# Kernel tuning notes

Hardware: AMD Instinct MI355X
Metric: run time of the kernel (lower is better)

Reference implementation:

```python
import jax, jax.numpy as jnp
import numpy as np

N_NODES = 40000
N_EDGES = 640000
N_GRAPHS = 256


def gcn_conv(x, W, b, src, dst, deg_inv_sqrt):
    # GCNConv: D^{-1/2} (A + I) D^{-1/2} X W + b
    h = (x @ W) * deg_inv_sqrt[:, None]          # pre-scale by norm of source
    agg = jax.ops.segment_sum(h[src], dst, num_segments=x.shape[0])
    agg = agg + h                                 # self-loop contribution
    return agg * deg_inv_sqrt[:, None] + b


def setup_inputs() -> dict:
    key = jax.random.key(0)
    ks = jax.random.split(key, 12)
    x = jax.random.normal(ks[0], (N_NODES, 128), dtype=jnp.float32)
    edge_index = jax.random.randint(ks[1], (2, N_EDGES), 0, N_NODES, dtype=jnp.int64)
    batch = jnp.sort(jax.random.randint(ks[2], (N_NODES,), 0, N_GRAPHS, dtype=jnp.int64))

    def glorot(k, shape):
        lim = float(np.sqrt(6.0 / (shape[0] + shape[1])))
        return jax.random.uniform(k, shape, jnp.float32, -lim, lim)

    return {
        "x": x,
        "W1": glorot(ks[3], (128, 128)), "b1": jnp.zeros((128,), jnp.float32),
        "W2": glorot(ks[4], (128, 64)),  "b2": jnp.zeros((64,), jnp.float32),
        "W3": glorot(ks[5], (64, 32)),   "b3": jnp.zeros((32,), jnp.float32),
        "Wl": glorot(ks[6], (32, 768)),  "bl": jnp.zeros((768,), jnp.float32),
        "edge_index": edge_index,
        "batch": batch,
    }


def reference(x, W1, b1, W2, b2, W3, b3, Wl, bl, edge_index, batch):
    n = x.shape[0]
    src, dst = edge_index[0], edge_index[1]
    # degree including self-loop (PyG gcn_norm with add_self_loops=True)
    deg = jax.ops.segment_sum(jnp.ones_like(dst, dtype=x.dtype), dst, num_segments=n) + 1.0
    dis = jax.lax.rsqrt(deg)

    h = jax.nn.relu(gcn_conv(x, W1, b1, src, dst, dis))
    h = jax.nn.relu(gcn_conv(h, W2, b2, src, dst, dis))
    h = jax.nn.relu(gcn_conv(h, W3, b3, src, dst, dis))

    # global mean pool per graph
    counts = jax.ops.segment_sum(jnp.ones((n,), x.dtype), batch, num_segments=N_GRAPHS)
    pooled = jax.ops.segment_sum(h, batch, num_segments=N_GRAPHS)
    pooled = pooled / jnp.maximum(counts, 1.0)[:, None]

    out = pooled @ Wl + bl                        # [B, 768]
    return out.reshape(N_GRAPHS, 48, 16)          # [B, 3*S^2, c]
```

## Files before the change

kernel.cpp:

```cpp
#include <hip/hip_runtime.h>
#include <hip/hip_fp16.h>


#define MAXSLOT 64

struct H8 { __half2 a, b, c, d; };

__device__ inline void acc_h8(float* acc, const H8& v) {
    float2 f;
    f = __half22float2(v.a); acc[0] += f.x; acc[1] += f.y;
    f = __half22float2(v.b); acc[2] += f.x; acc[3] += f.y;
    f = __half22float2(v.c); acc[4] += f.x; acc[5] += f.y;
    f = __half22float2(v.d); acc[6] += f.x; acc[7] += f.y;
}

__global__ void bucket_fill_kernel(const int* __restrict__ src, const int* __restrict__ dst,
                                   int* __restrict__ cursor, unsigned short* __restrict__ slots,
                                   int E) {
    int e = blockIdx.x * blockDim.x + threadIdx.x;
    if (e < E) {
        const int d = dst[e];
        const int pos = atomicAdd(&cursor[d], 1);
        if (pos < MAXSLOT) slots[(size_t)d * MAXSLOT + pos] = (unsigned short)src[e];
    }
}

template <int K, int C, int NR, bool HALF_IN>
__global__ __launch_bounds__(256, 4) void gemm_kernel(
        const void* __restrict__ x_, const float* __restrict__ W,
        const int* __restrict__ cursor, __half* __restrict__ h, int N) {
    constexpr int TC     = C / 8;
    constexpr int TN     = 256 / TC;
    constexpr int NPB    = NR * TN;
    constexpr int KSTAGE = 32;
    constexpr int XROW   = KSTAGE + 4;
    constexpr int WROW   = TC * 12;
    __shared__ __align__(16) float Xs[NPB * XROW];
    __shared__ __align__(16) float Ws[KSTAGE * WROW];

    const int tc = threadIdx.x % TC;
    const int tn = threadIdx.x / TC;
    const int c0 = tc * 8;
    const int nBase = blockIdx.x * NPB;
    const int n0 = nBase + tn * NR;

    float acc[NR][8] = {};

#pragma unroll 1
    for (int ks = 0; ks < K; ks += KSTAGE) {
        for (int idx = threadIdx.x; idx < KSTAGE * (C / 4); idx += 256) {
            const int k  = idx / (C / 4);
            const int f4 = idx % (C / 4);
            const int t  = f4 >> 1;
            const int hh = f4 & 1;
            *reinterpret_cast<float4*>(&Ws[k * WROW + t * 12 + hh * 4]) =
                *reinterpret_cast<const float4*>(&W[(size_t)(ks + k) * C + t * 8 + hh * 4]);
        }
        if (HALF_IN) {
            const __half* xh = (const __half*)x_;
            for (int idx = threadIdx.x; idx < NPB * (KSTAGE / 8); idx += 256) {
                const int row = idx / (KSTAGE / 8);
                const int c8  = (idx % (KSTAGE / 8)) * 8;
                const int nn  = nBase + row;
                float f[8];
                if (nn < N) {
                    const H8 v = *reinterpret_cast<const H8*>(&xh[(size_t)nn * K + ks + c8]);
                    float2 t2;
                    t2 = __half22float2(v.a); f[0] = t2.x; f[1] = t2.y;
                    t2 = __half22float2(v.b); f[2] = t2.x; f[3] = t2.y;
                    t2 = __half22float2(v.c); f[4] = t2.x; f[5] = t2.y;
                    t2 = __half22float2(v.d); f[6] = t2.x; f[7] = t2.y;
                } else {
#pragma unroll
                    for (int j = 0; j < 8; ++j) f[j] = 0.0f;
                }
                *reinterpret_cast<float4*>(&Xs[row * XROW + c8])     = *reinterpret_cast<float4*>(&f[0]);
                *reinterpret_cast<float4*>(&Xs[row * XROW + c8 + 4]) = *reinterpret_cast<float4*>(&f[4]);
            }
        } else {
            const float* xf = (const float*)x_;
            for (int idx = threadIdx.x; idx < NPB * (KSTAGE / 4); idx += 256) {
                const int row = idx / (KSTAGE / 4);
                const int c4  = (idx % (KSTAGE / 4)) * 4;
                const int nn  = nBase + row;
                const float4 v = (nn < N)
                    ? *reinterpret_cast<const float4*>(&xf[(size_t)nn * K + ks + c4])
                    : float4{0.f, 0.f, 0.f, 0.f};
                *reinterpret_cast<float4*>(&Xs[row * XROW + c4]) = v;
            }
        }
        __syncthreads();

#pragma unroll 2
        for (int k = 0; k < KSTAGE; k += 4) {
            float4 xv[NR];
#pragma unroll
            for (int i = 0; i < NR; ++i)
                xv[i] = *reinterpret_cast<const float4*>(&Xs[(tn * NR + i) * XROW + k]);
#pragma unroll
            for (int kk = 0; kk < 4; ++kk) {
                float wv[8];
                *reinterpret_cast<float4*>(&wv[0]) =
                    *reinterpret_cast<const float4*>(&Ws[(k + kk) * WROW + tc * 12]);
                *reinterpret_cast<float4*>(&wv[4]) =
                    *reinterpret_cast<const float4*>(&Ws[(k + kk) * WROW + tc * 12 + 4]);
#pragma unroll
                for (int i = 0; i < NR; ++i) {
                    const float xs = (&xv[i].x)[kk];
#pragma unroll
                    for (int j = 0; j < 8; ++j) acc[i][j] = fmaf(xs, wv[j], acc[i][j]);
                }
            }
        }
        __syncthreads();
    }

#pragma unroll
    for (int i = 0; i < NR; ++i) {
        const int nn = n0 + i;
        if (nn < N) {
            const float d = rsqrtf((float)cursor[nn] + 1.0f);
            H8 o;
            o.a = __floats2half2_rn(acc[i][0] * d, acc[i][1] * d);
            o.b = __floats2half2_rn(acc[i][2] * d, acc[i][3] * d);
            o.c = __floats2half2_rn(acc[i][4] * d, acc[i][5] * d);
            o.d = __floats2half2_rn(acc[i][6] * d, acc[i][7] * d);
            *reinterpret_cast<H8*>(&h[(size_t)nn * C + c0]) = o;
        }
    }
}

template <int C>
__global__ void gather_kernel(const __half* __restrict__ h, const int* __restrict__ cursor,
                              const unsigned short* __restrict__ slots,
                              const float* __restrict__ b, __half* __restrict__ outp, int N) {
    constexpr int CQ = C / 8;
    const long long tid = (long long)blockIdx.x * blockDim.x + threadIdx.x;
    const int node = (int)(tid / CQ);
    const int q    = (int)(tid % CQ);
    if (node >= N) return;

    const int degc = min(cursor[node], MAXSLOT);
    const unsigned short* sl = &slots[(size_t)node * MAXSLOT];

    float acc[8] = {};
    acc_h8(acc, *reinterpret_cast<const H8*>(&h[(size_t)node * C + q * 8]));

    int i = 0;
    for (; i + 8 <= degc; i += 8) {
        int s[8];
#pragma unroll
        for (int u = 0; u < 8; ++u) s[u] = sl[i + u];
        H8 v[8];
#pragma unroll
        for (int u = 0; u < 8; ++u) v[u] = *reinterpret_cast<const H8*>(&h[(size_t)s[u] * C + q * 8]);
#pragma unroll
        for (int u = 0; u < 8; ++u) acc_h8(acc, v[u]);
    }
    for (; i < degc; ++i) {
        const int s = sl[i];
        acc_h8(acc, *reinterpret_cast<const H8*>(&h[(size_t)s * C + q * 8]));
    }

    const float d = rsqrtf((float)cursor[node] + 1.0f);
    float r[8];
#pragma unroll
    for (int j = 0; j < 8; ++j) {
        float v = fmaf(acc[j], d, b[q * 8 + j]);
        r[j] = v > 0.0f ? v : 0.0f;
    }
    H8 o;
    o.a = __floats2half2_rn(r[0], r[1]);
    o.b = __floats2half2_rn(r[2], r[3]);
    o.c = __floats2half2_rn(r[4], r[5]);
    o.d = __floats2half2_rn(r[6], r[7]);
    *reinterpret_cast<H8*>(&outp[(size_t)node * C + q * 8]) = o;
}

__global__ __launch_bounds__(256) void gatherpoolhead_kernel(
        const __half* __restrict__ h, const int* __restrict__ cursor,
        const unsigned short* __restrict__ slots, const float* __restrict__ b3,
        const int* __restrict__ batch,
        const float* __restrict__ Wl, const float* __restrict__ bl,
        float* __restrict__ out, int N) {
    constexpr int C = 32;
    const int g = blockIdx.x;
    __shared__ int bounds[2];
    __shared__ __align__(16) float red[64 * 33];
    __shared__ float p[32];

    if (threadIdx.x == 0) {
        int lo = 0, hi = N;
        while (lo < hi) { int m = (lo + hi) >> 1; if (batch[m] <  g) lo = m + 1; else hi = m; }
        bounds[0] = lo;
        int lo2 = lo, hi2 = N;
        while (lo2 < hi2) { int m = (lo2 + hi2) >> 1; if (batch[m] <= g) lo2 = m + 1; else hi2 = m; }
        bounds[1] = lo2;
    }
    __syncthreads();
    const int lo = bounds[0], hi = bounds[1];

    const int q  = threadIdx.x & 3;
    const int nl = threadIdx.x >> 2;

    float pool[8] = {};
    for (int n = lo + nl; n < hi; n += 64) {
        const int degc = min(cursor[n], MAXSLOT);
        const unsigned short* sl = &slots[(size_t)n * MAXSLOT];

        float acc[8] = {};
        acc_h8(acc, *reinterpret_cast<const H8*>(&h[(size_t)n * C + q * 8]));
        int i = 0;
        for (; i + 4 <= degc; i += 4) {
            const int s0 = sl[i], s1 = sl[i + 1], s2 = sl[i + 2], s3 = sl[i + 3];
            const H8 v0 = *reinterpret_cast<const H8*>(&h[(size_t)s0 * C + q * 8]);
            const H8 v1 = *reinterpret_cast<const H8*>(&h[(size_t)s1 * C + q * 8]);
            const H8 v2 = *reinterpret_cast<const H8*>(&h[(size_t)s2 * C + q * 8]);
            const H8 v3 = *reinterpret_cast<const H8*>(&h[(size_t)s3 * C + q * 8]);
            acc_h8(acc, v0); acc_h8(acc, v1); acc_h8(acc, v2); acc_h8(acc, v3);
        }
        for (; i < degc; ++i) {
            const int s = sl[i];
            acc_h8(acc, *reinterpret_cast<const H8*>(&h[(size_t)s * C + q * 8]));
        }
        const float d = rsqrtf((float)cursor[n] + 1.0f);
#pragma unroll
        for (int j = 0; j < 8; ++j) {
            float v = fmaf(acc[j], d, b3[q * 8 + j]);
            pool[j] += v > 0.0f ? v : 0.0f;
        }
    }

#pragma unroll
    for (int j = 0; j < 8; ++j) red[nl * 33 + q * 8 + j] = pool[j];
    __syncthreads();
    for (int s = 32; s > 0; s >>= 1) {
        if (nl < s) {
#pragma unroll
            for (int j = 0; j < 8; ++j)
                red[nl * 33 + q * 8 + j] += red[(nl + s) * 33 + q * 8 + j];
        }
        __syncthreads();
    }
    if (threadIdx.x < 32) {
        float cnt = (float)(hi - lo);
        cnt = cnt < 1.0f ? 1.0f : cnt;
        p[threadIdx.x] = red[threadIdx.x] / cnt;
    }
    __syncthreads();

    for (int j = threadIdx.x; j < 768; j += 256) {
        float a = bl[j];
#pragma unroll
        for (int k = 0; k < 32; ++k) a = fmaf(p[k], Wl[k * 768 + j], a);
        out[g * 768 + j] = a;
    }
}


extern "C" void kernel_launch(void* const* d_in, const int* in_sizes, int n_in,
                              void* d_out, int out_size, void* d_ws, size_t ws_size,
                              hipStream_t stream) {
    const float* x   = (const float*)d_in[0];
    const float* W1  = (const float*)d_in[1];
    const float* b1  = (const float*)d_in[2];
    const float* W2  = (const float*)d_in[3];
    const float* b2  = (const float*)d_in[4];
    const float* W3  = (const float*)d_in[5];
    const float* b3  = (const float*)d_in[6];
    const float* Wl  = (const float*)d_in[7];
    const float* bl  = (const float*)d_in[8];
    const int* ei    = (const int*)d_in[9];
    const int* batch = (const int*)d_in[10];

    const int N = in_sizes[0] / 128;
    const int E = in_sizes[9] / 2;
    const int G = out_size / 768;

    const int* src = ei;
    const int* dst = ei + E;
    float* out = (float*)d_out;

    __half* H              = (__half*)d_ws;
    __half* A              = H + (size_t)N * 128;
    __half* Bb             = A + (size_t)N * 128;
    int* cursor            = (int*)(Bb + (size_t)N * 64);
    unsigned short* slots  = (unsigned short*)(cursor + N);

    hipMemsetAsync(cursor, 0, (size_t)N * sizeof(int), stream);
    bucket_fill_kernel<<<(E + 255) / 256, 256, 0, stream>>>(src, dst, cursor, slots, E);

    gemm_kernel<128, 128, 4, false><<<(N + 63) / 64, 256, 0, stream>>>(x, W1, cursor, H, N);
    gather_kernel<128><<<(int)(((long long)N * 16 + 255) / 256), 256, 0, stream>>>(
        H, cursor, slots, b1, A, N);

    gemm_kernel<128, 64, 2, true><<<(N + 63) / 64, 256, 0, stream>>>(A, W2, cursor, H, N);
    gather_kernel<64><<<(int)(((long long)N * 8 + 255) / 256), 256, 0, stream>>>(
        H, cursor, slots, b2, Bb, N);

    gemm_kernel<64, 32, 2, true><<<(N + 127) / 128, 256, 0, stream>>>(Bb, W3, cursor, H, N);

    gatherpoolhead_kernel<<<G, 256, 0, stream>>>(H, cursor, slots, b3, batch, Wl, bl, out, N);
}
```

Baseline: 240.4 us.

## Fuse bucket fill with layer-1 GEMM and fuse gathers with following GEMMs

Edge bucketing and the first X·W1 GEMM now share a single launch, with block ranges split between the two jobs. Because the degree is no longer known when the GEMM runs, the source normalization moves into the layer-1 gather as a per-neighbor rsqrt. The layer-1 and layer-2 gathers are fused with the next layer's small GEMM through shared-memory rows, which removes the intermediate activation round-trips to global memory and two launches. The slot table is halved to 32 entries and backed by a global overflow list that high-degree nodes scan linearly; this also makes the code handle degrees above the old cap correctly. The costs are extra per-neighbor cursor reads and a weaker per-thread GEMM inside the fused kernels.

```diff
diff --git a/kernel.cpp b/kernel.cpp
--- a/kernel.cpp
+++ b/kernel.cpp
@@ -2,7 +2,8 @@
 #include <hip/hip_fp16.h>
 
 
-#define MAXSLOT 64
+#define MAXSLOT 32
+#define OVFCAP  8192
 
 struct H8 { __half2 a, b, c, d; };
 
@@ -13,90 +14,75 @@
     f = __half22float2(v.c); acc[4] += f.x; acc[5] += f.y;
     f = __half22float2(v.d); acc[6] += f.x; acc[7] += f.y;
 }
-
-__global__ void bucket_fill_kernel(const int* __restrict__ src, const int* __restrict__ dst,
-                                   int* __restrict__ cursor, unsigned short* __restrict__ slots,
-                                   int E) {
-    int e = blockIdx.x * blockDim.x + threadIdx.x;
-    if (e < E) {
-        const int d = dst[e];
-        const int pos = atomicAdd(&cursor[d], 1);
-        if (pos < MAXSLOT) slots[(size_t)d * MAXSLOT + pos] = (unsigned short)src[e];
-    }
-}
-
-template <int K, int C, int NR, bool HALF_IN>
-__global__ __launch_bounds__(256, 4) void gemm_kernel(
-        const void* __restrict__ x_, const float* __restrict__ W,
-        const int* __restrict__ cursor, __half* __restrict__ h, int N) {
-    constexpr int TC     = C / 8;
-    constexpr int TN     = 256 / TC;
-    constexpr int NPB    = NR * TN;
-    constexpr int KSTAGE = 32;
-    constexpr int XROW   = KSTAGE + 4;
-    constexpr int WROW   = TC * 12;
-    __shared__ __align__(16) float Xs[NPB * XROW];
+__device__ inline void acc_h8s(float* acc, const H8& v, float s) {
+    float2 f;
+    f = __half22float2(v.a); acc[0] = fmaf(s, f.x, acc[0]); acc[1] = fmaf(s, f.y, acc[1]);
+    f = __half22float2(v.b); acc[2] = fmaf(s, f.x, acc[2]); acc[3] = fmaf(s, f.y, acc[3]);
+    f = __half22float2(v.c); acc[4] = fmaf(s, f.x, acc[4]); acc[5] = fmaf(s, f.y, acc[5]);
+    f = __half22float2(v.d); acc[6] = fmaf(s, f.x, acc[6]); acc[7] = fmaf(s, f.y, acc[7]);
+}
+
+__global__ __launch_bounds__(256, 4) void k1_kernel(
+        const int* __restrict__ src, const int* __restrict__ dst,
+        int* __restrict__ cursor, unsigned short* __restrict__ slots,
+        unsigned int* __restrict__ ovf, int* __restrict__ ovf_cnt,
+        const float* __restrict__ x, const float* __restrict__ W1,
+        __half* __restrict__ H1, int N, int E, int nBucket) {
+    constexpr int KSTAGE = 32, XROW = 36, WROW = 192;
+    __shared__ __align__(16) float Xs[64 * XROW];
     __shared__ __align__(16) float Ws[KSTAGE * WROW];
 
-    const int tc = threadIdx.x % TC;
-    const int tn = threadIdx.x / TC;
+    if ((int)blockIdx.x < nBucket) {
+        const int e = blockIdx.x * 256 + threadIdx.x;
+        if (e < E) {
+            const int d = dst[e];
+            const int pos = atomicAdd(&cursor[d], 1);
+            if (pos < MAXSLOT) {
+                slots[(size_t)d * MAXSLOT + pos] = (unsigned short)src[e];
+            } else {
+                const int o = atomicAdd(ovf_cnt, 1);
+                if (o < OVFCAP) ovf[o] = ((unsigned)d << 16) | (unsigned)src[e];
+            }
+        }
+        return;
+    }
+
+    const int tile = blockIdx.x - nBucket;
+    const int tc = threadIdx.x % 16;
+    const int tn = threadIdx.x / 16;
     const int c0 = tc * 8;
-    const int nBase = blockIdx.x * NPB;
-    const int n0 = nBase + tn * NR;
-
-    float acc[NR][8] = {};
+    const int nBase = tile * 64;
+    const int n0 = nBase + tn * 4;
+
+    float acc[4][8] = {};
 
 #pragma unroll 1
-    for (int ks = 0; ks < K; ks += KSTAGE) {
-        for (int idx = threadIdx.x; idx < KSTAGE * (C / 4); idx += 256) {
-            const int k  = idx / (C / 4);
-            const int f4 = idx % (C / 4);
+    for (int ks = 0; ks < 128; ks += KSTAGE) {
+        for (int idx = threadIdx.x; idx < KSTAGE * 32; idx += 256) {
+            const int k  = idx / 32;
+            const int f4 = idx % 32;
             const int t  = f4 >> 1;
             const int hh = f4 & 1;
             *reinterpret_cast<float4*>(&Ws[k * WROW + t * 12 + hh * 4]) =
-                *reinterpret_cast<const float4*>(&W[(size_t)(ks + k) * C + t * 8 + hh * 4]);
-        }
-        if (HALF_IN) {
-            const __half* xh = (const __half*)x_;
-            for (int idx = threadIdx.x; idx < NPB * (KSTAGE / 8); idx += 256) {
-                const int row = idx / (KSTAGE / 8);
-                const int c8  = (idx % (KSTAGE / 8)) * 8;
-                const int nn  = nBase + row;
-                float f[8];
-                if (nn < N) {
-                    const H8 v = *reinterpret_cast<const H8*>(&xh[(size_t)nn * K + ks + c8]);
-                    float2 t2;
-                    t2 = __half22float2(v.a); f[0] = t2.x; f[1] = t2.y;
-                    t2 = __half22float2(v.b); f[2] = t2.x; f[3] = t2.y;
-                    t2 = __half22float2(v.c); f[4] = t2.x; f[5] = t2.y;
-                    t2 = __half22float2(v.d); f[6] = t2.x; f[7] = t2.y;
-                } else {
-#pragma unroll
-                    for (int j = 0; j < 8; ++j) f[j] = 0.0f;
-                }
-                *reinterpret_cast<float4*>(&Xs[row * XROW + c8])     = *reinterpret_cast<float4*>(&f[0]);
-                *reinterpret_cast<float4*>(&Xs[row * XROW + c8 + 4]) = *reinterpret_cast<float4*>(&f[4]);
-            }
-        } else {
-            const float* xf = (const float*)x_;
-            for (int idx = threadIdx.x; idx < NPB * (KSTAGE / 4); idx += 256) {
-                const int row = idx / (KSTAGE / 4);
-                const int c4  = (idx % (KSTAGE / 4)) * 4;
-                const int nn  = nBase + row;
-                const float4 v = (nn < N)
-                    ? *reinterpret_cast<const float4*>(&xf[(size_t)nn * K + ks + c4])
-                    : float4{0.f, 0.f, 0.f, 0.f};
-                *reinterpret_cast<float4*>(&Xs[row * XROW + c4]) = v;
-            }
+                *reinterpret_cast<const float4*>(&W1[(size_t)(ks + k) * 128 + t * 8 + hh * 4]);
+        }
+        for (int idx = threadIdx.x; idx < 64 * (KSTAGE / 4); idx += 256) {
+            const int row = idx / (KSTAGE / 4);
+            const int c4  = (idx % (KSTAGE / 4)) * 4;
+            const int nn  = nBase + row;
+            const float4 v = (nn < N)
+                ? *reinterpret_cast<const float4*>(&x[(size_t)nn * 128 + ks + c4])
+                : float4{0.f, 0.f, 0.f, 0.f};
+            *reinterpret_cast<float4*>(&Xs[row * XROW + c4]) = v;
         }
         __syncthreads();
 
 #pragma unroll 2
         for (int k = 0; k < KSTAGE; k += 4) {
-            float4 xv[NR];
-#pragma unroll
-            for (int i = 0; i < NR; ++i)
-                xv[i] = *reinterpret_cast<const float4*>(&Xs[(tn * NR + i) * XROW + k]);
+            float4 xv[4];
+#pragma unroll
+            for (int i = 0; i < 4; ++i)
+                xv[i] = *reinterpret_cast<const float4*>(&Xs[(tn * 4 + i) * XROW + k]);
 #pragma unroll
             for (int kk = 0; kk < 4; ++kk) {
                 float wv[8];
@@ -105,7 +91,7 @@
                 *reinterpret_cast<float4*>(&wv[4]) =
                     *reinterpret_cast<const float4*>(&Ws[(k + kk) * WROW + tc * 12 + 4]);
 #pragma unroll
-                for (int i = 0; i < NR; ++i) {
+                for (int i = 0; i < 4; ++i) {
                     const float xs = (&xv[i].x)[kk];
 #pragma unroll
                     for (int j = 0; j < 8; ++j) acc[i][j] = fmaf(xs, wv[j], acc[i][j]);
@@ -116,74 +102,201 @@
     }
 
 #pragma unroll
-    for (int i = 0; i < NR; ++i) {
+    for (int i = 0; i < 4; ++i) {
         const int nn = n0 + i;
         if (nn < N) {
-            const float d = rsqrtf((float)cursor[nn] + 1.0f);
             H8 o;
-            o.a = __floats2half2_rn(acc[i][0] * d, acc[i][1] * d);
-            o.b = __floats2half2_rn(acc[i][2] * d, acc[i][3] * d);
-            o.c = __floats2half2_rn(acc[i][4] * d, acc[i][5] * d);
-            o.d = __floats2half2_rn(acc[i][6] * d, acc[i][7] * d);
-            *reinterpret_cast<H8*>(&h[(size_t)nn * C + c0]) = o;
-        }
-    }
-}
-
-template <int C>
-__global__ void gather_kernel(const __half* __restrict__ h, const int* __restrict__ cursor,
-                              const unsigned short* __restrict__ slots,
-                              const float* __restrict__ b, __half* __restrict__ outp, int N) {
-    constexpr int CQ = C / 8;
-    const long long tid = (long long)blockIdx.x * blockDim.x + threadIdx.x;
-    const int node = (int)(tid / CQ);
-    const int q    = (int)(tid % CQ);
-    if (node >= N) return;
-
-    const int degc = min(cursor[node], MAXSLOT);
-    const unsigned short* sl = &slots[(size_t)node * MAXSLOT];
-
-    float acc[8] = {};
-    acc_h8(acc, *reinterpret_cast<const H8*>(&h[(size_t)node * C + q * 8]));
-
-    int i = 0;
-    for (; i + 8 <= degc; i += 8) {
-        int s[8];
-#pragma unroll
-        for (int u = 0; u < 8; ++u) s[u] = sl[i + u];
-        H8 v[8];
-#pragma unroll
-        for (int u = 0; u < 8; ++u) v[u] = *reinterpret_cast<const H8*>(&h[(size_t)s[u] * C + q * 8]);
-#pragma unroll
-        for (int u = 0; u < 8; ++u) acc_h8(acc, v[u]);
-    }
-    for (; i < degc; ++i) {
-        const int s = sl[i];
-        acc_h8(acc, *reinterpret_cast<const H8*>(&h[(size_t)s * C + q * 8]));
-    }
-
-    const float d = rsqrtf((float)cursor[node] + 1.0f);
-    float r[8];
-#pragma unroll
-    for (int j = 0; j < 8; ++j) {
-        float v = fmaf(acc[j], d, b[q * 8 + j]);
-        r[j] = v > 0.0f ? v : 0.0f;
-    }
-    H8 o;
-    o.a = __floats2half2_rn(r[0], r[1]);
-    o.b = __floats2half2_rn(r[2], r[3]);
-    o.c = __floats2half2_rn(r[4], r[5]);
-    o.d = __floats2half2_rn(r[6], r[7]);
-    *reinterpret_cast<H8*>(&outp[(size_t)node * C + q * 8]) = o;
-}
-
-__global__ __launch_bounds__(256) void gatherpoolhead_kernel(
+            o.a = __floats2half2_rn(acc[i][0], acc[i][1]);
+            o.b = __floats2half2_rn(acc[i][2], acc[i][3]);
+            o.c = __floats2half2_rn(acc[i][4], acc[i][5]);
+            o.d = __floats2half2_rn(acc[i][6], acc[i][7]);
+            *reinterpret_cast<H8*>(&H1[(size_t)nn * 128 + c0]) = o;
+        }
+    }
+}
+
+__global__ __launch_bounds__(256, 4) void fuse12_kernel(
+        const __half* __restrict__ H1, const int* __restrict__ cursor,
+        const unsigned short* __restrict__ slots,
+        const unsigned int* __restrict__ ovf, const int* __restrict__ ovf_cnt,
+        const float* __restrict__ b1, const float* __restrict__ W2,
+        __half* __restrict__ H2, int N) {
+    __shared__ __half2 Wsh[128 * 32];
+    __shared__ __align__(16) float rows[16][132];
+
+    for (int i = threadIdx.x; i < 128 * 32; i += 256) {
+        const float2 w = *reinterpret_cast<const float2*>(&W2[i * 2]);
+        Wsh[i] = __floats2half2_rn(w.x, w.y);
+    }
+
+    const int ng = threadIdx.x >> 4;
+    const int q  = threadIdx.x & 15;
+    const int ntiles = (N + 15) / 16;
+
+    for (int t = blockIdx.x; t < ntiles; t += gridDim.x) {
+        const int node = t * 16 + ng;
+        if (node < N) {
+            const int deg = cursor[node];
+            const int m = min(deg, MAXSLOT);
+            const unsigned short* sl = &slots[(size_t)node * MAXSLOT];
+            const float dn = rsqrtf((float)deg + 1.0f);
+            float acc[8];
+            {
+                const H8 v = *reinterpret_cast<const H8*>(&H1[(size_t)node * 128 + q * 8]);
+                float2 f;
+                f = __half22float2(v.a); acc[0] = dn * f.x; acc[1] = dn * f.y;
+                f = __half22float2(v.b); acc[2] = dn * f.x; acc[3] = dn * f.y;
+                f = __half22float2(v.c); acc[4] = dn * f.x; acc[5] = dn * f.y;
+                f = __half22float2(v.d); acc[6] = dn * f.x; acc[7] = dn * f.y;
+            }
+            int i = 0;
+            for (; i + 4 <= m; i += 4) {
+                const int s0 = sl[i], s1 = sl[i + 1], s2 = sl[i + 2], s3 = sl[i + 3];
+                const float d0 = rsqrtf((float)cursor[s0] + 1.0f);
+                const float d1 = rsqrtf((float)cursor[s1] + 1.0f);
+                const float d2 = rsqrtf((float)cursor[s2] + 1.0f);
+                const float d3 = rsqrtf((float)cursor[s3] + 1.0f);
+                const H8 v0 = *reinterpret_cast<const H8*>(&H1[(size_t)s0 * 128 + q * 8]);
+                const H8 v1 = *reinterpret_cast<const H8*>(&H1[(size_t)s1 * 128 + q * 8]);
+                const H8 v2 = *reinterpret_cast<const H8*>(&H1[(size_t)s2 * 128 + q * 8]);
+                const H8 v3 = *reinterpret_cast<const H8*>(&H1[(size_t)s3 * 128 + q * 8]);
+                acc_h8s(acc, v0, d0); acc_h8s(acc, v1, d1);
+                acc_h8s(acc, v2, d2); acc_h8s(acc, v3, d3);
+            }
+            for (; i < m; ++i) {
+                const int s = sl[i];
+                const float ds = rsqrtf((float)cursor[s] + 1.0f);
+                acc_h8s(acc, *reinterpret_cast<const H8*>(&H1[(size_t)s * 128 + q * 8]), ds);
+            }
+            if (deg > MAXSLOT) {
+                const int oc = min(*ovf_cnt, OVFCAP);
+                for (int o = 0; o < oc; ++o) {
+                    const unsigned e = ovf[o];
+                    if ((int)(e >> 16) == node) {
+                        const int s = (int)(e & 0xffffu);
+                        const float ds = rsqrtf((float)cursor[s] + 1.0f);
+                        acc_h8s(acc, *reinterpret_cast<const H8*>(&H1[(size_t)s * 128 + q * 8]), ds);
+                    }
+                }
+            }
+#pragma unroll
+            for (int j = 0; j < 8; ++j) {
+                const float v = fmaf(acc[j], dn, b1[q * 8 + j]);
+                rows[ng][q * 8 + j] = v > 0.0f ? v : 0.0f;
+            }
+        } else {
+#pragma unroll
+            for (int j = 0; j < 8; ++j) rows[ng][q * 8 + j] = 0.0f;
+        }
+        __syncthreads();
+
+        {
+            float a0 = 0.f, a1 = 0.f, a2 = 0.f, a3 = 0.f;
+            for (int k = 0; k < 128; ++k) {
+                const float rk = rows[ng][k];
+                const float2 f01 = __half22float2(Wsh[k * 32 + q * 2]);
+                const float2 f23 = __half22float2(Wsh[k * 32 + q * 2 + 1]);
+                a0 = fmaf(rk, f01.x, a0); a1 = fmaf(rk, f01.y, a1);
+                a2 = fmaf(rk, f23.x, a2); a3 = fmaf(rk, f23.y, a3);
+            }
+            if (node < N) {
+                const float dn = rsqrtf((float)cursor[node] + 1.0f);
+                *reinterpret_cast<__half2*>(&H2[(size_t)node * 64 + q * 4]) =
+                    __floats2half2_rn(dn * a0, dn * a1);
+                *reinterpret_cast<__half2*>(&H2[(size_t)node * 64 + q * 4 + 2]) =
+                    __floats2half2_rn(dn * a2, dn * a3);
+            }
+        }
+        __syncthreads();
+    }
+}
+
+__global__ __launch_bounds__(256, 4) void fuse23_kernel(
+        const __half* __restrict__ H2, const int* __restrict__ cursor,
+        const unsigned short* __restrict__ slots,
+        const unsigned int* __restrict__ ovf, const int* __restrict__ ovf_cnt,
+        const float* __restrict__ b2, const float* __restrict__ W3,
+        __half* __restrict__ H3, int N) {
+    __shared__ __align__(16) float Ws3[64 * 32];
+    __shared__ float rows[32][66];
+
+    for (int i = threadIdx.x * 4; i < 64 * 32; i += 256 * 4)
+        *reinterpret_cast<float4*>(&Ws3[i]) = *reinterpret_cast<const float4*>(&W3[i]);
+
+    const int ng = threadIdx.x >> 3;
+    const int q  = threadIdx.x & 7;
+    const int ntiles = (N + 31) / 32;
+
+    for (int t = blockIdx.x; t < ntiles; t += gridDim.x) {
+        const int node = t * 32 + ng;
+        if (node < N) {
+            const int deg = cursor[node];
+            const int m = min(deg, MAXSLOT);
+            const unsigned short* sl = &slots[(size_t)node * MAXSLOT];
+            float acc[8] = {};
+            acc_h8(acc, *reinterpret_cast<const H8*>(&H2[(size_t)node * 64 + q * 8]));
+            int i = 0;
+            for (; i + 4 <= m; i += 4) {
+                const int s0 = sl[i], s1 = sl[i + 1], s2 = sl[i + 2], s3 = sl[i + 3];
+                const H8 v0 = *reinterpret_cast<const H8*>(&H2[(size_t)s0 * 64 + q * 8]);
+                const H8 v1 = *reinterpret_cast<const H8*>(&H2[(size_t)s1 * 64 + q * 8]);
+                const H8 v2 = *reinterpret_cast<const H8*>(&H2[(size_t)s2 * 64 + q * 8]);
+                const H8 v3 = *reinterpret_cast<const H8*>(&H2[(size_t)s3 * 64 + q * 8]);
+                acc_h8(acc, v0); acc_h8(acc, v1); acc_h8(acc, v2); acc_h8(acc, v3);
+            }
+            for (; i < m; ++i)
+                acc_h8(acc, *reinterpret_cast<const H8*>(&H2[(size_t)sl[i] * 64 + q * 8]));
+            if (deg > MAXSLOT) {
+                const int oc = min(*ovf_cnt, OVFCAP);
+                for (int o = 0; o < oc; ++o) {
+                    const unsigned e = ovf[o];
+                    if ((int)(e >> 16) == node)
+                        acc_h8(acc, *reinterpret_cast<const H8*>(&H2[(size_t)(e & 0xffffu) * 64 + q * 8]));
+                }
+            }
+            const float dn = rsqrtf((float)deg + 1.0f);
+#pragma unroll
+            for (int j = 0; j < 8; j += 2) {
+                float v0 = fmaf(acc[j],     dn, b2[q * 8 + j]);
+                float v1 = fmaf(acc[j + 1], dn, b2[q * 8 + j + 1]);
+                v0 = v0 > 0.0f ? v0 : 0.0f;
+                v1 = v1 > 0.0f ? v1 : 0.0f;
+                *reinterpret_cast<float2*>(&rows[ng][q * 8 + j]) = float2{v0, v1};
+            }
+        } else {
+#pragma unroll
+            for (int j = 0; j < 8; j += 2)
+                *reinterpret_cast<float2*>(&rows[ng][q * 8 + j]) = float2{0.f, 0.f};
+        }
+        __syncthreads();
+
+        {
+            float a0 = 0.f, a1 = 0.f, a2 = 0.f, a3 = 0.f;
+            for (int k = 0; k < 64; ++k) {
+                const float rk = rows[ng][k];
+                const float4 w = *reinterpret_cast<const float4*>(&Ws3[k * 32 + q * 4]);
+                a0 = fmaf(rk, w.x, a0); a1 = fmaf(rk, w.y, a1);
+                a2 = fmaf(rk, w.z, a2); a3 = fmaf(rk, w.w, a3);
+            }
+            if (node < N) {
+                const float dn = rsqrtf((float)cursor[node] + 1.0f);
+                *reinterpret_cast<__half2*>(&H3[(size_t)node * 32 + q * 4]) =
+                    __floats2half2_rn(dn * a0, dn * a1);
+                *reinterpret_cast<__half2*>(&H3[(size_t)node * 32 + q * 4 + 2]) =
+                    __floats2half2_rn(dn * a2, dn * a3);
+            }
+        }
+        __syncthreads();
+    }
+}
+
+__global__ __launch_bounds__(256) void gph_kernel(
         const __half* __restrict__ h, const int* __restrict__ cursor,
-        const unsigned short* __restrict__ slots, const float* __restrict__ b3,
-        const int* __restrict__ batch,
+        const unsigned short* __restrict__ slots,
+        const unsigned int* __restrict__ ovf, const int* __restrict__ ovf_cnt,
+        const float* __restrict__ b3, const int* __restrict__ batch,
         const float* __restrict__ Wl, const float* __restrict__ bl,
         float* __restrict__ out, int N) {
-    constexpr int C = 32;
     const int g = blockIdx.x;
     __shared__ int bounds[2];
     __shared__ __align__(16) float red[64 * 33];
@@ -205,28 +318,34 @@
 
     float pool[8] = {};
     for (int n = lo + nl; n < hi; n += 64) {
-        const int degc = min(cursor[n], MAXSLOT);
+        const int deg = cursor[n];
+        const int m = min(deg, MAXSLOT);
         const unsigned short* sl = &slots[(size_t)n * MAXSLOT];
-
         float acc[8] = {};
-        acc_h8(acc, *reinterpret_cast<const H8*>(&h[(size_t)n * C + q * 8]));
+        acc_h8(acc, *reinterpret_cast<const H8*>(&h[(size_t)n * 32 + q * 8]));
         int i = 0;
-        for (; i + 4 <= degc; i += 4) {
+        for (; i + 4 <= m; i += 4) {
             const int s0 = sl[i], s1 = sl[i + 1], s2 = sl[i + 2], s3 = sl[i + 3];
-            const H8 v0 = *reinterpret_cast<const H8*>(&h[(size_t)s0 * C + q * 8]);
-            const H8 v1 = *reinterpret_cast<const H8*>(&h[(size_t)s1 * C + q * 8]);
-            const H8 v2 = *reinterpret_cast<const H8*>(&h[(size_t)s2 * C + q * 8]);
-            const H8 v3 = *reinterpret_cast<const H8*>(&h[(size_t)s3 * C + q * 8]);
+            const H8 v0 = *reinterpret_cast<const H8*>(&h[(size_t)s0 * 32 + q * 8]);
+            const H8 v1 = *reinterpret_cast<const H8*>(&h[(size_t)s1 * 32 + q * 8]);
+            const H8 v2 = *reinterpret_cast<const H8*>(&h[(size_t)s2 * 32 + q * 8]);
+            const H8 v3 = *reinterpret_cast<const H8*>(&h[(size_t)s3 * 32 + q * 8]);
             acc_h8(acc, v0); acc_h8(acc, v1); acc_h8(acc, v2); acc_h8(acc, v3);
         }
-        for (; i < degc; ++i) {
-            const int s = sl[i];
-            acc_h8(acc, *reinterpret_cast<const H8*>(&h[(size_t)s * C + q * 8]));
-        }
-        const float d = rsqrtf((float)cursor[n] + 1.0f);
+        for (; i < m; ++i)
+            acc_h8(acc, *reinterpret_cast<const H8*>(&h[(size_t)sl[i] * 32 + q * 8]));
+        if (deg > MAXSLOT) {
+            const int oc = min(*ovf_cnt, OVFCAP);
+            for (int o = 0; o < oc; ++o) {
+                const unsigned e = ovf[o];
+                if ((int)(e >> 16) == n)
+                    acc_h8(acc, *reinterpret_cast<const H8*>(&h[(size_t)(e & 0xffffu) * 32 + q * 8]));
+            }
+        }
+        const float d = rsqrtf((float)deg + 1.0f);
 #pragma unroll
         for (int j = 0; j < 8; ++j) {
-            float v = fmaf(acc[j], d, b3[q * 8 + j]);
+            const float v = fmaf(acc[j], d, b3[q * 8 + j]);
             pool[j] += v > 0.0f ? v : 0.0f;
         }
     }
@@ -281,24 +400,28 @@
     const int* dst = ei + E;
     float* out = (float*)d_out;
 
-    __half* H              = (__half*)d_ws;
-    __half* A              = H + (size_t)N * 128;
-    __half* Bb             = A + (size_t)N * 128;
-    int* cursor            = (int*)(Bb + (size_t)N * 64);
-    unsigned short* slots  = (unsigned short*)(cursor + N);
-
-    hipMemsetAsync(cursor, 0, (size_t)N * sizeof(int), stream);
-    bucket_fill_kernel<<<(E + 255) / 256, 256, 0, stream>>>(src, dst, cursor, slots, E);
-
-    gemm_kernel<128, 128, 4, false><<<(N + 63) / 64, 256, 0, stream>>>(x, W1, cursor, H, N);
-    gather_kernel<128><<<(int)(((long long)N * 16 + 255) / 256), 256, 0, stream>>>(
-        H, cursor, slots, b1, A, N);
-
-    gemm_kernel<128, 64, 2, true><<<(N + 63) / 64, 256, 0, stream>>>(A, W2, cursor, H, N);
-    gather_kernel<64><<<(int)(((long long)N * 8 + 255) / 256), 256, 0, stream>>>(
-        H, cursor, slots, b2, Bb, N);
-
-    gemm_kernel<64, 32, 2, true><<<(N + 127) / 128, 256, 0, stream>>>(Bb, W3, cursor, H, N);
-
-    gatherpoolhead_kernel<<<G, 256, 0, stream>>>(H, cursor, slots, b3, batch, Wl, bl, out, N);
-}
+    __half* H1             = (__half*)d_ws;
+    __half* H2             = H1 + (size_t)N * 128;
+    __half* H3             = H2 + (size_t)N * 64;
+    int* cursor            = (int*)(H3 + (size_t)N * 32);
+    int* ovf_cnt           = cursor + N;
+    unsigned int* ovf      = (unsigned int*)(ovf_cnt + 1);
+    unsigned short* slots  = (unsigned short*)(ovf + OVFCAP);
+
+    const int nBucket = (E + 255) / 256;
+    const int nGemm1  = (N + 63) / 64;
+
+    hipMemsetAsync(cursor, 0, (size_t)(N + 1) * sizeof(int), stream);
+
+    k1_kernel<<<nBucket + nGemm1, 256, 0, stream>>>(
+        src, dst, cursor, slots, ovf, ovf_cnt, x, W1, H1, N, E, nBucket);
+
+    fuse12_kernel<<<1024, 256, 0, stream>>>(
+        H1, cursor, slots, ovf, ovf_cnt, b1, W2, H2, N);
+
+    fuse23_kernel<<<1024, 256, 0, stream>>>(
+        H2, cursor, slots, ovf, ovf_cnt, b2, W3, H3, N);
+
+    gph_kernel<<<G, 256, 0, stream>>>(
+        H3, cursor, slots, ovf, ovf_cnt, b3, batch, Wl, bl, out, N);
+}
```

Result: no change. 237.2 us (-1.4%).
